# Kernel optimization log

Hardware: AMD Instinct MI355X
Metric: run time of the kernel (lower is better)

The kernel has to match this reference:

```python
import math
import jax, jax.numpy as jnp
import numpy as np

B, T, C = 1, 4096, 1024
H, DH = 16, 64
BAND = 128

def setup_inputs() -> dict:
    key = jax.random.key(0)
    ks = jax.random.split(key, 5)
    scale = 0.02
    return {
        "x":  jax.random.normal(ks[0], (B, T, C), dtype=jnp.float32),
        "Wq": jax.random.normal(ks[1], (C, C), dtype=jnp.float32) * scale,
        "Wk": jax.random.normal(ks[2], (C, C), dtype=jnp.float32) * scale,
        "Wv": jax.random.normal(ks[3], (C, C), dtype=jnp.float32) * scale,
        "Wo": jax.random.normal(ks[4], (C, C), dtype=jnp.float32) * scale,
    }

def _band_causal_mask(T, band, dtype=jnp.bool_):
    # allowed iff j <= i and (i - j) < band
    i = jnp.arange(T)[:, None]
    j = jnp.arange(T)[None, :]
    return (j <= i) & ((i - j) < band)  # (T, T)

def reference(x, Wq, Wk, Wv, Wo):
    Bs, Ts, Cs = x.shape
    # nn.Linear: y = x @ W^T (bias=False)
    q = (x @ Wq.T).reshape(Bs, Ts, H, DH).transpose(0, 2, 1, 3)  # (B,H,T,Dh)
    k = (x @ Wk.T).reshape(Bs, Ts, H, DH).transpose(0, 2, 1, 3)
    v = (x @ Wv.T).reshape(Bs, Ts, H, DH).transpose(0, 2, 1, 3)
    att = jnp.einsum('bhid,bhjd->bhij', q, k) / math.sqrt(DH)      # (B,H,T,T)
    mask = _band_causal_mask(Ts, BAND)                              # (T,T)
    att = jnp.where(mask[None, None], att, jnp.finfo(att.dtype).min)
    P = jax.nn.softmax(att, axis=-1)
    y = jnp.einsum('bhij,bhjd->bhid', P, v)                         # (B,H,T,Dh)
    y = y.transpose(0, 2, 1, 3).reshape(Bs, Ts, Cs)                 # (B,T,C)
    return y @ Wo.T
```

## Files before the change

kernel.cpp:

```cpp
#include <hip/hip_runtime.h>
#include <hip/hip_bf16.h>
#include <stdint.h>

#define T_SEQ 4096
#define CDIM  1024
#define NH    16
#define DHEAD 64
#define BAND  128

typedef __bf16 bf16;
typedef __attribute__((ext_vector_type(8))) __bf16 bf16x8;
typedef __attribute__((ext_vector_type(4))) float  f32x4;

__device__ __forceinline__ void async_ld16(const bf16* g, bf16* l) {
    __builtin_amdgcn_global_load_lds(
        (__attribute__((address_space(1))) void*)g,
        (__attribute__((address_space(3))) void*)l, 16, 0, 0);
}

__global__ void cvt_all(const float* __restrict__ x,  const float* __restrict__ wq,
                        const float* __restrict__ wk, const float* __restrict__ wv,
                        const float* __restrict__ wo,
                        bf16* __restrict__ xb, bf16* __restrict__ wqkvb,
                        bf16* __restrict__ wob) {
    size_t g = (size_t)blockIdx.x * 256 + threadIdx.x;
    const float* s; bf16* d;
    if (g < 524288) {
        s = x + g * 8; d = xb + g * 8;
    } else if (g < 917504) {
        size_t i2 = (g - 524288) * 8;
        int which = (int)(i2 >> 20);
        s = ((which == 0) ? wq : (which == 1) ? wk : wv) + (i2 & 1048575);
        d = wqkvb + i2;
    } else {
        size_t i3 = (g - 917504) * 8;
        s = wo + i3; d = wob + i3;
    }
    const float4* sv = (const float4*)s;
    float4 a = sv[0], b = sv[1];
    bf16x8 o;
    o[0] = (bf16)a.x; o[1] = (bf16)a.y; o[2] = (bf16)a.z; o[3] = (bf16)a.w;
    o[4] = (bf16)b.x; o[5] = (bf16)b.y; o[6] = (bf16)b.z; o[7] = (bf16)b.w;
    *(bf16x8*)d = o;
}

__global__ __launch_bounds__(256) void gemm_qkv(
        const bf16* __restrict__ A, const bf16* __restrict__ B,
        bf16* __restrict__ qb, bf16* __restrict__ kb, bf16* __restrict__ vtb) {
    const int K = 1024;
    __shared__ __align__(16) bf16 lds_a[128 * 32];
    __shared__ __align__(16) bf16 lds_b[128 * 32];
    int t = threadIdx.x;
    int w = t >> 6, l = t & 63;
    int quad = l >> 4, col = l & 15;
    int bx = blockIdx.x;
    int bm = bx & 31, bn = bx >> 5;
    int m0 = bm * 128, n0 = bn * 128;
    int wm = (w >> 1) * 64, wn = (w & 1) * 64;

    f32x4 acc[4][4];
#pragma unroll
    for (int i = 0; i < 4; i++)
#pragma unroll
        for (int j = 0; j < 4; j++) acc[i][j] = (f32x4){0.f, 0.f, 0.f, 0.f};

    int c0 = t, c1 = 256 + t;
    int ra0 = c0 >> 2, ka0 = (c0 & 3) * 8;
    int ra1 = c1 >> 2, ka1 = (c1 & 3) * 8;
    bf16* la0 = lds_a + (size_t)(w * 64) * 8;
    bf16* la1 = lds_a + (size_t)(256 + w * 64) * 8;
    bf16* lb0 = lds_b + (size_t)(w * 64) * 8;
    bf16* lb1 = lds_b + (size_t)(256 + w * 64) * 8;

    for (int k0 = 0; k0 < K; k0 += 32) {
        async_ld16(A + (size_t)(m0 + ra0) * K + k0 + ka0, la0);
        async_ld16(A + (size_t)(m0 + ra1) * K + k0 + ka1, la1);
        async_ld16(B + (size_t)(n0 + ra0) * K + k0 + ka0, lb0);
        async_ld16(B + (size_t)(n0 + ra1) * K + k0 + ka1, lb1);
        __syncthreads();
        const bf16x8* pa = (const bf16x8*)lds_a;
        const bf16x8* pb = (const bf16x8*)lds_b;
        bf16x8 af[4], bfr[4];
#pragma unroll
        for (int i = 0; i < 4; i++) af[i]  = pa[(wm + i * 16 + col) * 4 + quad];
#pragma unroll
        for (int j = 0; j < 4; j++) bfr[j] = pb[(wn + j * 16 + col) * 4 + quad];
#pragma unroll
        for (int i = 0; i < 4; i++)
#pragma unroll
            for (int j = 0; j < 4; j++)
                acc[i][j] = __builtin_amdgcn_mfma_f32_16x16x32_bf16(af[i], bfr[j], acc[i][j], 0, 0, 0);
        __syncthreads();
    }
#pragma unroll
    for (int i = 0; i < 4; i++)
#pragma unroll
        for (int j = 0; j < 4; j++) {
            int mbase = m0 + wm + i * 16 + quad * 4;
            int ncol = n0 + wn + j * 16 + col;
            int which = ncol >> 10;
            int o = ncol & 1023;
            int h = o >> 6, d = o & 63;
#pragma unroll
            for (int r = 0; r < 4; r++) {
                int tt = mbase + r;
                bf16 v = (bf16)acc[i][j][r];
                if (which == 0)       qb[((size_t)(h * T_SEQ + tt)) * 64 + d] = v;
                else if (which == 1)  kb[((size_t)(h * T_SEQ + tt)) * 64 + d] = v;
                else                  vtb[((size_t)(h * 64 + d)) * T_SEQ + tt] = v;
            }
        }
}

#define PSTR 168

__global__ __launch_bounds__(256) void attn(
        const bf16* __restrict__ qbuf, const bf16* __restrict__ kbuf,
        const bf16* __restrict__ vtbuf, bf16* __restrict__ yb) {
    __shared__ __align__(16) bf16 p_lds[4 * 32 * PSTR];
    int t = threadIdx.x;
    int w = t >> 6, l = t & 63;
    int quad = l >> 4, col = l & 15;
    int h = blockIdx.x >> 5;
    int qt = blockIdx.x & 31;
    int i0 = qt * 128;
    int rowbase = i0 + w * 32;
    int jbase = rowbase - 128;

    const bf16* Q  = qbuf  + (size_t)h * T_SEQ * 64;
    const bf16* Kp = kbuf  + (size_t)h * T_SEQ * 64;
    const bf16* Vt = vtbuf + (size_t)h * 64 * T_SEQ;

    bf16x8 qf[2][2];
#pragma unroll
    for (int mi = 0; mi < 2; mi++)
#pragma unroll
        for (int kk = 0; kk < 2; kk++)
            qf[mi][kk] = *(const bf16x8*)(Q + (size_t)(rowbase + mi * 16 + col) * 64 + kk * 32 + quad * 8);

    f32x4 s[2][10];
#pragma unroll
    for (int mi = 0; mi < 2; mi++)
#pragma unroll
        for (int nj = 0; nj < 10; nj++) s[mi][nj] = (f32x4){0.f, 0.f, 0.f, 0.f};
#pragma unroll
    for (int nj = 0; nj < 10; nj++) {
        int jr = jbase + nj * 16 + col;
        int jl = jr < 0 ? 0 : jr;
#pragma unroll
        for (int kk = 0; kk < 2; kk++) {
            bf16x8 kf = *(const bf16x8*)(Kp + (size_t)jl * 64 + kk * 32 + quad * 8);
#pragma unroll
            for (int mi = 0; mi < 2; mi++)
                s[mi][nj] = __builtin_amdgcn_mfma_f32_16x16x32_bf16(qf[mi][kk], kf, s[mi][nj], 0, 0, 0);
        }
    }

    float l_run[2][4];
#pragma unroll
    for (int mi = 0; mi < 2; mi++)
#pragma unroll
        for (int r = 0; r < 4; r++) {
            int ii = rowbase + mi * 16 + quad * 4 + r;
            float mx = -3.0e38f;
#pragma unroll
            for (int nj = 0; nj < 10; nj++) {
                int jj = jbase + nj * 16 + col;
                bool ok = (jj >= 0) && ((unsigned)(ii - jj) < (unsigned)BAND);
                float v = ok ? s[mi][nj][r] * 0.125f : -3.0e38f;
                s[mi][nj][r] = v;
                mx = fmaxf(mx, v);
            }
            mx = fmaxf(mx, __shfl_xor(mx, 1));
            mx = fmaxf(mx, __shfl_xor(mx, 2));
            mx = fmaxf(mx, __shfl_xor(mx, 4));
            mx = fmaxf(mx, __shfl_xor(mx, 8));
            float rs = 0.f;
#pragma unroll
            for (int nj = 0; nj < 10; nj++) {
                float p = __expf(s[mi][nj][r] - mx);
                s[mi][nj][r] = p;
                rs += p;
            }
            rs += __shfl_xor(rs, 1);
            rs += __shfl_xor(rs, 2);
            rs += __shfl_xor(rs, 4);
            rs += __shfl_xor(rs, 8);
            l_run[mi][r] = rs;
        }

    bf16* myp = p_lds + (size_t)w * (32 * PSTR);
#pragma unroll
    for (int mi = 0; mi < 2; mi++)
#pragma unroll
        for (int nj = 0; nj < 10; nj++)
#pragma unroll
            for (int r = 0; r < 4; r++)
                myp[(mi * 16 + quad * 4 + r) * PSTR + nj * 16 + col] = (bf16)s[mi][nj][r];

    f32x4 o_acc[2][4];
#pragma unroll
    for (int mi = 0; mi < 2; mi++)
#pragma unroll
        for (int di = 0; di < 4; di++) o_acc[mi][di] = (f32x4){0.f, 0.f, 0.f, 0.f};
#pragma unroll
    for (int kj = 0; kj < 5; kj++) {
        int jv = jbase + kj * 32 + quad * 8;
        int jvc = jv < 0 ? 0 : jv;
        bf16x8 pf[2];
#pragma unroll
        for (int mi = 0; mi < 2; mi++)
            pf[mi] = *(const bf16x8*)(myp + (mi * 16 + col) * PSTR + kj * 32 + quad * 8);
#pragma unroll
        for (int di = 0; di < 4; di++) {
            bf16x8 vf = *(const bf16x8*)(Vt + (size_t)(di * 16 + col) * T_SEQ + jvc);
#pragma unroll
            for (int mi = 0; mi < 2; mi++)
                o_acc[mi][di] = __builtin_amdgcn_mfma_f32_16x16x32_bf16(pf[mi], vf, o_acc[mi][di], 0, 0, 0);
        }
    }

#pragma unroll
    for (int mi = 0; mi < 2; mi++)
#pragma unroll
        for (int di = 0; di < 4; di++)
#pragma unroll
            for (int r = 0; r < 4; r++) {
                int tt = rowbase + mi * 16 + quad * 4 + r;
                int c = h * 64 + di * 16 + col;
                yb[(size_t)tt * CDIM + c] = (bf16)(o_acc[mi][di][r] / l_run[mi][r]);
            }
}

__global__ __launch_bounds__(256) void gemm_proj(
        const bf16* __restrict__ A, const bf16* __restrict__ B,
        float* __restrict__ Cout) {
    const int K = 1024;
    __shared__ __align__(16) bf16 lds_a[64 * 32];
    __shared__ __align__(16) bf16 lds_b[128 * 32];
    int t = threadIdx.x;
    int w = t >> 6, l = t & 63;
    int quad = l >> 4, col = l & 15;
    int bx = blockIdx.x;
    int bm = bx & 63, bn = bx >> 6;
    int m0 = bm * 64, n0 = bn * 128;
    int wm = (w >> 1) * 32, wn = (w & 1) * 64;

    f32x4 acc[2][4];
#pragma unroll
    for (int i = 0; i < 2; i++)
#pragma unroll
        for (int j = 0; j < 4; j++) acc[i][j] = (f32x4){0.f, 0.f, 0.f, 0.f};

    int ra0 = t >> 2, ka0 = (t & 3) * 8;
    int c1 = t, c2 = 256 + t;
    int rb1 = c1 >> 2, kb1 = (c1 & 3) * 8;
    int rb2 = c2 >> 2, kb2 = (c2 & 3) * 8;
    bf16* la0 = lds_a + (size_t)(w * 64) * 8;
    bf16* lb1 = lds_b + (size_t)(w * 64) * 8;
    bf16* lb2 = lds_b + (size_t)(256 + w * 64) * 8;

    for (int k0 = 0; k0 < K; k0 += 32) {
        async_ld16(A + (size_t)(m0 + ra0) * K + k0 + ka0, la0);
        async_ld16(B + (size_t)(n0 + rb1) * K + k0 + kb1, lb1);
        async_ld16(B + (size_t)(n0 + rb2) * K + k0 + kb2, lb2);
        __syncthreads();
        const bf16x8* pa = (const bf16x8*)lds_a;
        const bf16x8* pb = (const bf16x8*)lds_b;
        bf16x8 af[2], bfr[4];
#pragma unroll
        for (int i = 0; i < 2; i++) af[i]  = pa[(wm + i * 16 + col) * 4 + quad];
#pragma unroll
        for (int j = 0; j < 4; j++) bfr[j] = pb[(wn + j * 16 + col) * 4 + quad];
#pragma unroll
        for (int i = 0; i < 2; i++)
#pragma unroll
            for (int j = 0; j < 4; j++)
                acc[i][j] = __builtin_amdgcn_mfma_f32_16x16x32_bf16(af[i], bfr[j], acc[i][j], 0, 0, 0);
        __syncthreads();
    }
#pragma unroll
    for (int i = 0; i < 2; i++)
#pragma unroll
        for (int j = 0; j < 4; j++) {
            int mbase = m0 + wm + i * 16 + quad * 4;
            int ncol = n0 + wn + j * 16 + col;
#pragma unroll
            for (int r = 0; r < 4; r++)
                Cout[(size_t)(mbase + r) * CDIM + ncol] = acc[i][j][r];
        }
}

extern "C" void kernel_launch(void* const* d_in, const int* in_sizes, int n_in,
                              void* d_out, int out_size, void* d_ws, size_t ws_size,
                              hipStream_t stream) {
    const float* x  = (const float*)d_in[0];
    const float* Wq = (const float*)d_in[1];
    const float* Wk = (const float*)d_in[2];
    const float* Wv = (const float*)d_in[3];
    const float* Wo = (const float*)d_in[4];
    float* out = (float*)d_out;

    char* ws = (char*)d_ws;
    bf16* xb    = (bf16*)(ws);
    bf16* wqkvb = (bf16*)(ws + ((size_t)8  << 20));
    bf16* wob   = (bf16*)(ws + ((size_t)14 << 20));
    bf16* qb    = (bf16*)(ws + ((size_t)16 << 20));
    bf16* kb    = (bf16*)(ws + ((size_t)24 << 20));
    bf16* vtb   = (bf16*)(ws + ((size_t)32 << 20));
    bf16* yb    = (bf16*)(ws + ((size_t)40 << 20));

    cvt_all<<<4096, 256, 0, stream>>>(x, Wq, Wk, Wv, Wo, xb, wqkvb, wob);
    gemm_qkv<<<768, 256, 0, stream>>>(xb, wqkvb, qb, kb, vtb);
    attn<<<512, 256, 0, stream>>>(qb, kb, vtb, yb);
    gemm_proj<<<512, 256, 0, stream>>>(yb, wob, out);
}
```

Before: 155.9 us.

## Fold softmax scale into Q, transpose V via LDS, move Wo cast into attention

The QKV GEMM epilogue now multiplies Q by 1/sqrt(d)*log2(e), so attention can use exp2 without a per-score multiply. V^T is staged through LDS so it is written to global memory in coalesced 16-byte rows instead of strided scalar stores. The attention kernel now runs 128-thread blocks over 64-row query tiles, giving twice as many blocks, and each block also converts a slice of Wo to bf16, which removes that work from the conversion kernel. Smaller attention tiles reload K/V bands with more overlap between neighbouring blocks.

Measured after the change: 162.8 us. +4.5%, slower.

```diff
diff --git a/kernel.cpp b/kernel.cpp
--- a/kernel.cpp
+++ b/kernel.cpp
@@ -10,7 +10,10 @@
 
 typedef __bf16 bf16;
 typedef __attribute__((ext_vector_type(8))) __bf16 bf16x8;
+typedef __attribute__((ext_vector_type(4))) __bf16 bf16x4;
 typedef __attribute__((ext_vector_type(4))) float  f32x4;
+
+#define QSCALE 0.1803368801111204f
 
 __device__ __forceinline__ void async_ld16(const bf16* g, bf16* l) {
     __builtin_amdgcn_global_load_lds(
@@ -20,21 +23,16 @@
 
 __global__ void cvt_all(const float* __restrict__ x,  const float* __restrict__ wq,
                         const float* __restrict__ wk, const float* __restrict__ wv,
-                        const float* __restrict__ wo,
-                        bf16* __restrict__ xb, bf16* __restrict__ wqkvb,
-                        bf16* __restrict__ wob) {
+                        bf16* __restrict__ xb, bf16* __restrict__ wqkvb) {
     size_t g = (size_t)blockIdx.x * 256 + threadIdx.x;
     const float* s; bf16* d;
     if (g < 524288) {
         s = x + g * 8; d = xb + g * 8;
-    } else if (g < 917504) {
+    } else {
         size_t i2 = (g - 524288) * 8;
         int which = (int)(i2 >> 20);
         s = ((which == 0) ? wq : (which == 1) ? wk : wv) + (i2 & 1048575);
         d = wqkvb + i2;
-    } else {
-        size_t i3 = (g - 917504) * 8;
-        s = wo + i3; d = wob + i3;
     }
     const float4* sv = (const float4*)s;
     float4 a = sv[0], b = sv[1];
@@ -48,8 +46,9 @@
         const bf16* __restrict__ A, const bf16* __restrict__ B,
         bf16* __restrict__ qb, bf16* __restrict__ kb, bf16* __restrict__ vtb) {
     const int K = 1024;
-    __shared__ __align__(16) bf16 lds_a[128 * 32];
-    __shared__ __align__(16) bf16 lds_b[128 * 32];
+    __shared__ __align__(16) bf16 smem[8192];
+    bf16* lds_a = smem;
+    bf16* lds_b = smem + 4096;
     int t = threadIdx.x;
     int w = t >> 6, l = t & 63;
     int quad = l >> 4, col = l & 15;
@@ -92,38 +91,81 @@
                 acc[i][j] = __builtin_amdgcn_mfma_f32_16x16x32_bf16(af[i], bfr[j], acc[i][j], 0, 0, 0);
         __syncthreads();
     }
-#pragma unroll
-    for (int i = 0; i < 4; i++)
-#pragma unroll
-        for (int j = 0; j < 4; j++) {
-            int mbase = m0 + wm + i * 16 + quad * 4;
-            int ncol = n0 + wn + j * 16 + col;
-            int which = ncol >> 10;
-            int o = ncol & 1023;
-            int h = o >> 6, d = o & 63;
-#pragma unroll
-            for (int r = 0; r < 4; r++) {
-                int tt = mbase + r;
-                bf16 v = (bf16)acc[i][j][r];
-                if (which == 0)       qb[((size_t)(h * T_SEQ + tt)) * 64 + d] = v;
-                else if (which == 1)  kb[((size_t)(h * T_SEQ + tt)) * 64 + d] = v;
-                else                  vtb[((size_t)(h * 64 + d)) * T_SEQ + tt] = v;
-            }
-        }
+
+    if (n0 < 2048) {
+        bool isQ = (n0 < 1024);
+        bf16* dst = isQ ? qb : kb;
+        float scale = isQ ? QSCALE : 1.0f;
+        int obase = n0 & 1023;
+#pragma unroll
+        for (int i = 0; i < 4; i++)
+#pragma unroll
+            for (int j = 0; j < 4; j++) {
+                int mbase = m0 + wm + i * 16 + quad * 4;
+                int o = obase + wn + j * 16 + col;
+                int h = o >> 6, d = o & 63;
+#pragma unroll
+                for (int r = 0; r < 4; r++)
+                    dst[((size_t)(h * T_SEQ + mbase + r)) * 64 + d] =
+                        (bf16)(acc[i][j][r] * scale);
+            }
+    } else {
+        int obase = n0 - 2048;
+        bf16* tb = smem;
+#pragma unroll
+        for (int c = 0; c < 4; c++) {
+            __syncthreads();
+            if ((w & 1) == (c >> 1)) {
+                int jlo = 2 * (c & 1);
+#pragma unroll
+                for (int i = 0; i < 4; i++)
+#pragma unroll
+                    for (int jj = 0; jj < 2; jj++) {
+                        int j = jlo + jj;
+                        int nl = jj * 16 + col;
+                        int mb = wm + i * 16 + quad * 4;
+                        bf16x4 pk;
+#pragma unroll
+                        for (int r = 0; r < 4; r++) pk[r] = (bf16)acc[i][j][r];
+                        *(bf16x4*)(tb + nl * 136 + mb) = pk;
+                    }
+            }
+            __syncthreads();
+#pragma unroll
+            for (int rd = 0; rd < 2; rd++) {
+                int nrow = rd * 16 + w * 4 + (l >> 4);
+                int moff = (l & 15) * 8;
+                bf16x8 vrow = *(const bf16x8*)(tb + nrow * 136 + moff);
+                *(bf16x8*)(vtb + (size_t)(obase + c * 32 + nrow) * T_SEQ + m0 + moff) = vrow;
+            }
+        }
+    }
 }
 
 #define PSTR 168
 
-__global__ __launch_bounds__(256) void attn(
+__global__ __launch_bounds__(128) void attn(
         const bf16* __restrict__ qbuf, const bf16* __restrict__ kbuf,
-        const bf16* __restrict__ vtbuf, bf16* __restrict__ yb) {
-    __shared__ __align__(16) bf16 p_lds[4 * 32 * PSTR];
+        const bf16* __restrict__ vtbuf, bf16* __restrict__ yb,
+        const float* __restrict__ wo, bf16* __restrict__ wob) {
+    __shared__ __align__(16) bf16 p_lds[2 * 32 * PSTR];
     int t = threadIdx.x;
     int w = t >> 6, l = t & 63;
     int quad = l >> 4, col = l & 15;
-    int h = blockIdx.x >> 5;
-    int qt = blockIdx.x & 31;
-    int i0 = qt * 128;
+
+    {
+        size_t g = ((size_t)blockIdx.x * 128 + t) * 8;
+        const float4* sv = (const float4*)(wo + g);
+        float4 a = sv[0], b = sv[1];
+        bf16x8 o8;
+        o8[0] = (bf16)a.x; o8[1] = (bf16)a.y; o8[2] = (bf16)a.z; o8[3] = (bf16)a.w;
+        o8[4] = (bf16)b.x; o8[5] = (bf16)b.y; o8[6] = (bf16)b.z; o8[7] = (bf16)b.w;
+        *(bf16x8*)(wob + g) = o8;
+    }
+
+    int h = blockIdx.x >> 6;
+    int qt = blockIdx.x & 63;
+    int i0 = qt * 64;
     int rowbase = i0 + w * 32;
     int jbase = rowbase - 128;
 
@@ -167,7 +209,7 @@
             for (int nj = 0; nj < 10; nj++) {
                 int jj = jbase + nj * 16 + col;
                 bool ok = (jj >= 0) && ((unsigned)(ii - jj) < (unsigned)BAND);
-                float v = ok ? s[mi][nj][r] * 0.125f : -3.0e38f;
+                float v = ok ? s[mi][nj][r] : -3.0e38f;
                 s[mi][nj][r] = v;
                 mx = fmaxf(mx, v);
             }
@@ -178,7 +220,7 @@
             float rs = 0.f;
 #pragma unroll
             for (int nj = 0; nj < 10; nj++) {
-                float p = __expf(s[mi][nj][r] - mx);
+                float p = __builtin_amdgcn_exp2f(s[mi][nj][r] - mx);
                 s[mi][nj][r] = p;
                 rs += p;
             }
@@ -310,8 +352,8 @@
     bf16* vtb   = (bf16*)(ws + ((size_t)32 << 20));
     bf16* yb    = (bf16*)(ws + ((size_t)40 << 20));
 
-    cvt_all<<<4096, 256, 0, stream>>>(x, Wq, Wk, Wv, Wo, xb, wqkvb, wob);
+    cvt_all<<<3584, 256, 0, stream>>>(x, Wq, Wk, Wv, xb, wqkvb);
     gemm_qkv<<<768, 256, 0, stream>>>(xb, wqkvb, qb, kb, vtb);
-    attn<<<512, 256, 0, stream>>>(qb, kb, vtb, yb);
+    attn<<<1024, 128, 0, stream>>>(qb, kb, vtb, yb, Wo, wob);
     gemm_proj<<<512, 256, 0, stream>>>(yb, wob, out);
 }
```
